# Optimization experiments

Hardware: AMD Instinct MI355X
Metric: run time of the kernel (lower is better)

## Reference

```python
import jax, jax.numpy as jnp
import numpy as np

N = 50000       # nodes
E = 800000      # edges
F_IN = 197      # node_feature_dim
H = 256         # hidden_dim
HEADS = 8
HD = H // HEADS # 32
L = 5           # num_layers
FF = 4 * H      # 1024
C = 2           # num_classes
ED = 2          # edge_feature_dim
SCALE = float(np.sqrt(HD))


def _ln(x, g, b):
    m = x.mean(-1, keepdims=True)
    v = ((x - m) ** 2).mean(-1, keepdims=True)
    return (x - m) / jnp.sqrt(v + 1e-5) * g + b


def setup_inputs() -> dict:
    key = jax.random.key(0)
    ks = iter(jax.random.split(key, 40))
    d = {}
    d["x"] = jax.random.normal(next(ks), (N, F_IN), dtype=jnp.float32)
    d["edge_index"] = jax.random.randint(next(ks), (2, E), 0, N, dtype=jnp.int64)
    d["edge_attr"] = jax.random.normal(next(ks), (E, ED), dtype=jnp.float32)
    xav = lambda k, sh: jax.random.normal(k, sh, dtype=jnp.float32) * float(np.sqrt(2.0 / (sh[-2] + sh[-1])))
    # input projection + LN
    d["in_W"] = xav(next(ks), (F_IN, H)); d["in_b"] = jnp.zeros((H,), jnp.float32)
    d["in_g"] = jnp.ones((H,), jnp.float32); d["in_bb"] = jnp.zeros((H,), jnp.float32)
    # stacked per-layer params (leading dim L)
    d["Wq"] = xav(next(ks), (L, H, H)); d["Wk"] = xav(next(ks), (L, H, H)); d["Wv"] = xav(next(ks), (L, H, H))
    d["We"] = xav(next(ks), (L, ED, HEADS)); d["be"] = jnp.zeros((L, HEADS), jnp.float32)
    d["Wo"] = xav(next(ks), (L, H, H)); d["bo"] = jnp.zeros((L, H), jnp.float32)
    d["ln1_g"] = jnp.ones((L, H), jnp.float32); d["ln1_b"] = jnp.zeros((L, H), jnp.float32)
    d["ln2_g"] = jnp.ones((L, H), jnp.float32); d["ln2_b"] = jnp.zeros((L, H), jnp.float32)
    d["f1_W"] = xav(next(ks), (L, H, FF)); d["f1_b"] = jnp.zeros((L, FF), jnp.float32)
    d["f2_W"] = xav(next(ks), (L, FF, H)); d["f2_b"] = jnp.zeros((L, H), jnp.float32)
    # classifier
    d["cls1_W"] = xav(next(ks), (H, H // 2)); d["cls1_b"] = jnp.zeros((H // 2,), jnp.float32)
    d["cls2_W"] = xav(next(ks), (H // 2, C)); d["cls2_b"] = jnp.zeros((C,), jnp.float32)
    return d


def _forward(x, edge_index, edge_attr, in_W, in_b, in_g, in_bb,
             Wq, Wk, Wv, We, be, Wo, bo, ln1_g, ln1_b, ln2_g, ln2_b,
             f1_W, f1_b, f2_W, f2_b, cls1_W, cls1_b, cls2_W, cls2_b):
    src, dst = edge_index[0], edge_index[1]  # message flows src -> dst
    h = jax.nn.gelu(_ln(x @ in_W + in_b, in_g, in_bb), approximate=False)

    def layer(h, p):
        wq, wk, wv, we, b_e, wo, b_o, g1, b1, g2, b2, w1, bf1, w2, bf2 = p
        hn = _ln(h, g1, b1)
        q = (hn @ wq).reshape(-1, HEADS, HD)
        k = (hn @ wk).reshape(-1, HEADS, HD)
        v = (hn @ wv).reshape(-1, HEADS, HD)
        edge_bias = edge_attr @ we + b_e                        # (E, HEADS)
        score = (q[dst] * k[src]).sum(-1) / SCALE + edge_bias   # (E, HEADS)
        # segment softmax over destination nodes
        mx = jax.ops.segment_max(score, dst, num_segments=N)
        mx = jnp.where(jnp.isfinite(mx), mx, 0.0)
        ex = jnp.exp(score - mx[dst])
        denom = jax.ops.segment_sum(ex, dst, num_segments=N)
        w = ex / (denom[dst] + 1e-16)                           # (E, HEADS)
        msg = w[:, :, None] * v[src]                            # (E, HEADS, HD)
        agg = jax.ops.segment_sum(msg.reshape(-1, H), dst, num_segments=N)
        out = agg @ wo + b_o
        out = _ln(out + h, g2, b2)                              # residual_proj = Identity
        ffn = jax.nn.gelu(out @ w1 + bf1, approximate=False) @ w2 + bf2
        return out + ffn, None

    params = (Wq, Wk, Wv, We, be, Wo, bo, ln1_g, ln1_b, ln2_g, ln2_b, f1_W, f1_b, f2_W, f2_b)
    h, _ = jax.lax.scan(layer, h, params)
    logits = jax.nn.gelu(h @ cls1_W + cls1_b, approximate=False) @ cls2_W + cls2_b
    probs = jax.nn.softmax(logits, axis=-1)
    return logits, probs


def reference(x, edge_index, edge_attr, in_W, in_b, in_g, in_bb,
              Wq, Wk, Wv, We, be, Wo, bo, ln1_g, ln1_b, ln2_g, ln2_b,
              f1_W, f1_b, f2_W, f2_b, cls1_W, cls1_b, cls2_W, cls2_b):
    return _forward(x, edge_index, edge_attr, in_W, in_b, in_g, in_bb,
                    Wq, Wk, Wv, We, be, Wo, bo, ln1_g, ln1_b, ln2_g, ln2_b,
                    f1_W, f1_b, f2_W, f2_b, cls1_W, cls1_b, cls2_W, cls2_b)
```

## Files before the change

kernel.cpp:

```cpp
#include <hip/hip_runtime.h>
#include <math.h>

#define NN 50000
#define NE 800000
#define FIN 197
#define KIN 224
#define H 256
#define HEADS 8
#define HD 32
#define LAYERS 5
#define FF 1024
#define INV_SCALE 0.17677669529663687f

typedef __attribute__((ext_vector_type(8))) short short8;
typedef __attribute__((ext_vector_type(4))) float f32x4;
typedef unsigned short ushort;

__device__ __forceinline__ float gelu_f(float x) {
    float x2 = x * x;
    float u = __builtin_fmaf(0.044715f * x2, x, x);
    float e = __builtin_amdgcn_exp2f(-2.3022075f * u);
    return x * __builtin_amdgcn_rcpf(1.0f + e);
}
__device__ __forceinline__ ushort f2b(float f) {
    unsigned u = __float_as_uint(f);
    u += 0x7fffu + ((u >> 16) & 1u);
    return (ushort)(u >> 16);
}
__device__ __forceinline__ float b2f(ushort b) {
    return __uint_as_float(((unsigned)b) << 16);
}
__device__ __forceinline__ float dot2b(unsigned a, unsigned b) {
    float a0 = __uint_as_float(a << 16), a1 = __uint_as_float(a & 0xffff0000u);
    float b0 = __uint_as_float(b << 16), b1 = __uint_as_float(b & 0xffff0000u);
    return a0 * b0 + a1 * b1;
}

__device__ __forceinline__ void load16_lds(const ushort* gp, ushort* lp) {
    __builtin_amdgcn_global_load_lds(
        (const __attribute__((address_space(1))) unsigned int*)gp,
        (__attribute__((address_space(3))) unsigned int*)lp,
        16, 0, 0);
}

__global__ __launch_bounds__(256) void gemm_bf16_kernel(
    const ushort* __restrict__ A, int lda,
    const ushort* __restrict__ Bt,
    const float* __restrict__ bias,
    const float* __restrict__ res, int ldr,
    float* __restrict__ Cf, ushort* __restrict__ Cb, int ldc,
    int n, int K, int act, int gx)
{
    __shared__ ushort As[2][128 * 32];
    __shared__ ushort Bs[2][64 * 32];
    int tid = threadIdx.x;
    int lane = tid & 63;
    int wave = tid >> 6;

    int tiles_y = (n + 127) >> 7;
    int lin = blockIdx.x;
    int gsz = gx * 8;
    int group = lin / gsz;
    int rem = lin - group * gsz;
    int rows_left = tiles_y - group * 8;
    int rg = rows_left < 8 ? rows_left : 8;
    int r = rem % rg;
    int c = rem / rg;
    int brow = (group * 8 + r) * 128;
    int bcol = c * 64;

    f32x4 acc[2][4] = {};
    int m0 = lane & 15;
    int rdc = ((lane >> 4) ^ ((lane >> 1) & 3)) * 8;

    int rA = lane >> 2;
    int c8s = (((lane & 3) ^ ((lane >> 3) & 3)) * 8);

    long arow0, arow1, brow0;
    {
        int gr0 = brow + wave * 32 + rA;        if (gr0 >= n) gr0 = n - 1;
        int gr1 = brow + wave * 32 + 16 + rA;   if (gr1 >= n) gr1 = n - 1;
        arow0 = (long)gr0 * lda;
        arow1 = (long)gr1 * lda;
        brow0 = (long)(bcol + wave * 16 + rA) * K;
    }
    int loA0 = (wave * 32) * 32;
    int loA1 = (wave * 32 + 16) * 32;
    int loB  = (wave * 16) * 32;

    int nt = K >> 5;
    load16_lds(A + arow0 + c8s, &As[0][loA0]);
    load16_lds(A + arow1 + c8s, &As[0][loA1]);
    load16_lds(Bt + brow0 + c8s, &Bs[0][loB]);
    __syncthreads();

    for (int t = 0; t < nt; ++t) {
        int p = t & 1;
        if (t + 1 < nt) {
            int k0 = (t + 1) << 5;
            load16_lds(A + arow0 + k0 + c8s, &As[p ^ 1][loA0]);
            load16_lds(A + arow1 + k0 + c8s, &As[p ^ 1][loA1]);
            load16_lds(Bt + brow0 + k0 + c8s, &Bs[p ^ 1][loB]);
        }
        short8 af[2], bfr[4];
        #pragma unroll
        for (int i = 0; i < 2; ++i)
            af[i] = *(const short8*)&As[p][(wave * 32 + i * 16 + m0) * 32 + rdc];
        #pragma unroll
        for (int j = 0; j < 4; ++j)
            bfr[j] = *(const short8*)&Bs[p][(j * 16 + m0) * 32 + rdc];
        #pragma unroll
        for (int i = 0; i < 2; ++i)
            #pragma unroll
            for (int j = 0; j < 4; ++j)
                acc[i][j] = __builtin_amdgcn_mfma_f32_16x16x32_bf16(af[i], bfr[j], acc[i][j], 0, 0, 0);
        __syncthreads();
    }

    float* ep0 = (float*)&As[0][wave * 1024];
    float* ep1 = (float*)&As[1][wave * 1024];
    int ccol = lane & 15;
    int crow0 = (lane >> 4) * 4;
    float* epw = (lane < 32) ? ep0 : ep1;
    #pragma unroll
    for (int i = 0; i < 2; ++i) {
        int rowbase = brow + wave * 32 + i * 16;
        #pragma unroll
        for (int rr = 0; rr < 4; ++rr) {
            int r8 = (crow0 + rr) & 7;
            #pragma unroll
            for (int j = 0; j < 4; ++j)
                epw[r8 * 64 + j * 16 + ccol] = acc[i][j][rr];
        }
        #pragma unroll
        for (int pass = 0; pass < 2; ++pass) {
            const float* ep = pass ? ep1 : ep0;
            #pragma unroll
            for (int k = 0; k < 2; ++k) {
                int idx = k * 64 + lane;
                int lr  = idx >> 4;
                int c4  = (idx & 15) * 4;
                int grow = rowbase + pass * 8 + lr;
                f32x4 v = *(const f32x4*)&ep[lr * 64 + c4];
                int gcol = bcol + c4;
                if (bias) {
                    float4 b4 = *(const float4*)(bias + gcol);
                    v[0] += b4.x; v[1] += b4.y; v[2] += b4.z; v[3] += b4.w;
                }
                if (act) {
                    v[0] = gelu_f(v[0]); v[1] = gelu_f(v[1]);
                    v[2] = gelu_f(v[2]); v[3] = gelu_f(v[3]);
                }
                if (grow < n) {
                    if (res) {
                        float4 r4 = *(const float4*)(res + (long)grow * ldr + gcol);
                        v[0] += r4.x; v[1] += r4.y; v[2] += r4.z; v[3] += r4.w;
                    }
                    if (Cf) *(f32x4*)(Cf + (long)grow * ldc + gcol) = v;
                    if (Cb) {
                        ushort4 ob = { f2b(v[0]), f2b(v[1]), f2b(v[2]), f2b(v[3]) };
                        *(ushort4*)(Cb + (long)grow * ldc + gcol) = ob;
                    }
                }
            }
        }
    }
}

__global__ __launch_bounds__(256) void ln256_kernel(
    const float* __restrict__ af, const ushort* __restrict__ ab,
    const float* __restrict__ res,
    const float* __restrict__ g, const float* __restrict__ bta,
    float* __restrict__ outf, ushort* __restrict__ outb, int n, int post_gelu)
{
    int row = blockIdx.x * 4 + (threadIdx.x >> 6);
    if (row >= n) return;
    int lane = threadIdx.x & 63;
    float4 v;
    if (af) {
        v = *(const float4*)(af + (long)row * H + lane * 4);
    } else {
        ushort4 vb = *(const ushort4*)(ab + (long)row * H + lane * 4);
        v.x = b2f(vb.x); v.y = b2f(vb.y); v.z = b2f(vb.z); v.w = b2f(vb.w);
    }
    if (res) {
        float4 r = *(const float4*)(res + (long)row * H + lane * 4);
        v.x += r.x; v.y += r.y; v.z += r.z; v.w += r.w;
    }
    float s = v.x + v.y + v.z + v.w;
    #pragma unroll
    for (int off = 1; off < 64; off <<= 1) s += __shfl_xor(s, off);
    float mean = s * (1.0f / H);
    float dx = v.x - mean, dy = v.y - mean, dz = v.z - mean, dw = v.w - mean;
    float qs = dx * dx + dy * dy + dz * dz + dw * dw;
    #pragma unroll
    for (int off = 1; off < 64; off <<= 1) qs += __shfl_xor(qs, off);
    float rstd = rsqrtf(qs * (1.0f / H) + 1e-5f);
    float4 gg = *(const float4*)(g + lane * 4);
    float4 bb = *(const float4*)(bta + lane * 4);
    float4 o;
    o.x = dx * rstd * gg.x + bb.x;
    o.y = dy * rstd * gg.y + bb.y;
    o.z = dz * rstd * gg.z + bb.z;
    o.w = dw * rstd * gg.w + bb.w;
    if (post_gelu) { o.x = gelu_f(o.x); o.y = gelu_f(o.y); o.z = gelu_f(o.z); o.w = gelu_f(o.w); }
    if (outf) *(float4*)(outf + (long)row * H + lane * 4) = o;
    if (outb) {
        ushort4 ob = { f2b(o.x), f2b(o.y), f2b(o.z), f2b(o.w) };
        *(ushort4*)(outb + (long)row * H + lane * 4) = ob;
    }
}

__global__ __launch_bounds__(256) void xcast_kernel(const float* __restrict__ x,
                                                    ushort* __restrict__ xb)
{
    long i = (long)blockIdx.x * 256 + threadIdx.x;
    if (i >= (long)NN * KIN) return;
    int n = (int)(i / KIN), c = (int)(i % KIN);
    xb[i] = (c < FIN) ? f2b(x[(long)n * FIN + c]) : (ushort)0;
}

__global__ __launch_bounds__(256) void wtin_kernel(const float* __restrict__ W,
                                                   ushort* __restrict__ Wt)
{
    int i = blockIdx.x * 256 + threadIdx.x;
    if (i >= 256 * KIN) return;
    int m = i / KIN, k = i % KIN;
    Wt[i] = (k < FIN) ? f2b(W[(long)k * H + m]) : (ushort)0;
}

__global__ __launch_bounds__(256) void wtqkv_kernel(
    const float* __restrict__ Wq, const float* __restrict__ Wk,
    const float* __restrict__ Wv, ushort* __restrict__ out)
{
    long i = (long)blockIdx.x * 256 + threadIdx.x;
    if (i >= (long)LAYERS * 768 * 256) return;
    int l = (int)(i / (768 * 256));
    int r = (int)(i % (768 * 256));
    int m = r >> 8, k = r & 255;
    const float* W = (m < 256) ? Wq : ((m < 512) ? Wk : Wv);
    out[i] = f2b(W[(long)l * 65536 + (long)k * 256 + (m & 255)]);
}

__global__ __launch_bounds__(256) void wtgen_kernel(
    const float* __restrict__ W, ushort* __restrict__ out, int L, int K, int M)
{
    long i = (long)blockIdx.x * 256 + threadIdx.x;
    if (i >= (long)L * K * M) return;
    int l = (int)(i / ((long)K * M));
    int r = (int)(i % ((long)K * M));
    int m = r / K, k = r % K;
    out[i] = f2b(W[(long)l * K * M + (long)k * M + m]);
}

__global__ __launch_bounds__(256) void deg_kernel(const int* __restrict__ dst,
                                                   int* __restrict__ deg)
{
    int e = blockIdx.x * 256 + threadIdx.x;
    if (e >= NE) return;
    atomicAdd(&deg[dst[e]], 1);
}

__global__ __launch_bounds__(256) void scan1_kernel(const int* __restrict__ deg,
                                                     int* __restrict__ rowptr,
                                                     int* __restrict__ bsum)
{
    __shared__ int buf[256];
    int tid = threadIdx.x;
    int i = blockIdx.x * 256 + tid;
    int v = (i < NN) ? deg[i] : 0;
    buf[tid] = v;
    __syncthreads();
    #pragma unroll
    for (int off = 1; off < 256; off <<= 1) {
        int t = (tid >= off) ? buf[tid - off] : 0;
        __syncthreads();
        buf[tid] += t;
        __syncthreads();
    }
    if (i < NN) rowptr[i] = buf[tid] - v;
    if (tid == 255) bsum[blockIdx.x] = buf[255];
}

__global__ __launch_bounds__(256) void scan2_kernel(int* __restrict__ bsum, int nb)
{
    __shared__ int buf[256];
    int tid = threadIdx.x;
    int v = (tid < nb) ? bsum[tid] : 0;
    buf[tid] = v;
    __syncthreads();
    #pragma unroll
    for (int off = 1; off < 256; off <<= 1) {
        int t = (tid >= off) ? buf[tid - off] : 0;
        __syncthreads();
        buf[tid] += t;
        __syncthreads();
    }
    if (tid < nb) bsum[tid] = buf[tid] - v;
}

__global__ __launch_bounds__(256) void scan3_kernel(int* __restrict__ rowptr,
                                                     const int* __restrict__ bsum)
{
    int i = blockIdx.x * 256 + threadIdx.x;
    if (i < NN) rowptr[i] += bsum[blockIdx.x];
    if (i == 0) rowptr[NN] = NE;
}

__global__ __launch_bounds__(256) void fill_kernel(
    const int* __restrict__ src, const int* __restrict__ dst,
    const float* __restrict__ ea, const int* __restrict__ rowptr,
    int* __restrict__ cursor, int* __restrict__ csr_src,
    float2* __restrict__ csr_ea)
{
    int e = blockIdx.x * 256 + threadIdx.x;
    if (e >= NE) return;
    int d = dst[e];
    int pos = atomicAdd(&cursor[d], 1);
    int j = rowptr[d] + pos;
    csr_src[j] = src[e];
    csr_ea[j] = *(const float2*)(ea + 2 * e);
}

#define LOADE(idx, kbuf, vbuf, ebuf)                                   \
    { int s_ = csr_src[idx]; ebuf = csr_ea[idx];                       \
      const ushort* kr_ = qkv + (long)s_ * 768 + 256;                  \
      kbuf = *(const uint2*)(kr_ + lane * 4);                          \
      vbuf = *(const uint2*)(kr_ + 256 + lane * 4); }

#define PAIR(k1, v1, e1, k2, v2, e2)                                               \
    { float p1 = dot2b(q2.x, (k1).x) + dot2b(q2.y, (k1).y);                        \
      float p2 = dot2b(q2.x, (k2).x) + dot2b(q2.y, (k2).y);                        \
      p1 += __shfl_xor(p1, 1);  p2 += __shfl_xor(p2, 1);                           \
      p1 += __shfl_xor(p1, 2);  p2 += __shfl_xor(p2, 2);                           \
      p1 += __shfl_xor(p1, 4);  p2 += __shfl_xor(p2, 4);                           \
      float s1 = p1 * c1 + (e1).x * w0 + (e1).y * w1 + bb;                         \
      float s2 = p2 * c1 + (e2).x * w0 + (e2).y * w1 + bb;                         \
      float mp = fmaxf(s1, s2);                                                    \
      float x1 = __builtin_amdgcn_exp2f(s1 - mp);                                  \
      float x2 = __builtin_amdgcn_exp2f(s2 - mp);                                  \
      float lp = x1 + x2;                                                          \
      float b0 = x1 * __uint_as_float((v1).x << 16)         + x2 * __uint_as_float((v2).x << 16);          \
      float b1 = x1 * __uint_as_float((v1).x & 0xffff0000u) + x2 * __uint_as_float((v2).x & 0xffff0000u);  \
      float b2 = x1 * __uint_as_float((v1).y << 16)         + x2 * __uint_as_float((v2).y << 16);          \
      float b3 = x1 * __uint_as_float((v1).y & 0xffff0000u) + x2 * __uint_as_float((v2).y & 0xffff0000u);  \
      float mn = fmaxf(m, mp);                                                     \
      float so = __builtin_amdgcn_exp2f(m - mn);                                   \
      float sp = __builtin_amdgcn_exp2f(mp - mn);                                  \
      l  = l  * so + lp * sp;                                                      \
      a0 = a0 * so + b0 * sp;                                                      \
      a1 = a1 * so + b1 * sp;                                                      \
      a2 = a2 * so + b2 * sp;                                                      \
      a3 = a3 * so + b3 * sp;                                                      \
      m = mn; }

#define SINGLE(kb, vb, eb)                                                         \
    { float p1 = dot2b(q2.x, (kb).x) + dot2b(q2.y, (kb).y);                        \
      p1 += __shfl_xor(p1, 1);                                                     \
      p1 += __shfl_xor(p1, 2);                                                     \
      p1 += __shfl_xor(p1, 4);                                                     \
      float s1 = p1 * c1 + (eb).x * w0 + (eb).y * w1 + bb;                         \
      float mn = fmaxf(m, s1);                                                     \
      float so = __builtin_amdgcn_exp2f(m - mn);                                   \
      float e_ = __builtin_amdgcn_exp2f(s1 - mn);                                  \
      l  = l  * so + e_;                                                           \
      a0 = a0 * so + e_ * __uint_as_float((vb).x << 16);                           \
      a1 = a1 * so + e_ * __uint_as_float((vb).x & 0xffff0000u);                   \
      a2 = a2 * so + e_ * __uint_as_float((vb).y << 16);                           \
      a3 = a3 * so + e_ * __uint_as_float((vb).y & 0xffff0000u);                   \
      m = mn; }

__global__ __launch_bounds__(256) void attn_kernel(
    const ushort* __restrict__ qkv,
    const int* __restrict__ rowptr, const int* __restrict__ csr_src,
    const float2* __restrict__ csr_ea,
    const float* __restrict__ We, const float* __restrict__ be,
    ushort* __restrict__ aggb)
{
    int node = blockIdx.x * 4 + (threadIdx.x >> 6);
    if (node >= NN) return;
    int lane = threadIdx.x & 63;
    int h = lane >> 3;
    const float L2E = 1.4426950408889634f;
    float w0 = We[h] * L2E, w1 = We[8 + h] * L2E, bb = be[h] * L2E;
    const float c1 = INV_SCALE * L2E;

    uint2 q2 = *(const uint2*)(qkv + (long)node * 768 + lane * 4);
    int jbeg = rowptr[node], jend = rowptr[node + 1];

    float m = -1e30f, l = 0.f;
    float a0 = 0.f, a1 = 0.f, a2 = 0.f, a3 = 0.f;

    uint2 k0v = {0,0}, v0v = {0,0}, k1v = {0,0}, v1v = {0,0};
    uint2 k2v = {0,0}, v2v = {0,0}, k3v = {0,0}, v3v = {0,0};
    float2 e0v = {0.f,0.f}, e1v = {0.f,0.f}, e2v = {0.f,0.f}, e3v = {0.f,0.f};

    if (jbeg + 0 < jend) LOADE(jbeg + 0, k0v, v0v, e0v);
    if (jbeg + 1 < jend) LOADE(jbeg + 1, k1v, v1v, e1v);
    if (jbeg + 2 < jend) LOADE(jbeg + 2, k2v, v2v, e2v);
    if (jbeg + 3 < jend) LOADE(jbeg + 3, k3v, v3v, e3v);

    int j = jbeg;
    for (; j + 3 < jend; j += 4) {
        PAIR(k0v, v0v, e0v, k1v, v1v, e1v);
        if (j + 4 < jend) LOADE(j + 4, k0v, v0v, e0v);
        if (j + 5 < jend) LOADE(j + 5, k1v, v1v, e1v);
        PAIR(k2v, v2v, e2v, k3v, v3v, e3v);
        if (j + 6 < jend) LOADE(j + 6, k2v, v2v, e2v);
        if (j + 7 < jend) LOADE(j + 7, k3v, v3v, e3v);
    }
    int rleft = jend - j;
    if (rleft >= 2) PAIR(k0v, v0v, e0v, k1v, v1v, e1v);
    if (rleft == 3) SINGLE(k2v, v2v, e2v);
    if (rleft == 1) SINGLE(k0v, v0v, e0v);

    float inv = 1.0f / (l + 1e-16f);
    ushort4 o = { f2b(a0 * inv), f2b(a1 * inv), f2b(a2 * inv), f2b(a3 * inv) };
    *(ushort4*)(aggb + (long)node * 256 + lane * 4) = o;
}

__global__ __launch_bounds__(256) void cls_kernel(
    const float* __restrict__ t1, const float* __restrict__ W,
    const float* __restrict__ b, float* __restrict__ out)
{
    int i = blockIdx.x * 256 + threadIdx.x;
    if (i >= NN) return;
    const float* tp = t1 + (long)i * 128;
    float a0 = 0.f, a1 = 0.f;
    #pragma unroll
    for (int j = 0; j < 128; j += 4) {
        float4 t = *(const float4*)(tp + j);
        a0 += t.x * W[(j + 0) * 2] + t.y * W[(j + 1) * 2] + t.z * W[(j + 2) * 2] + t.w * W[(j + 3) * 2];
        a1 += t.x * W[(j + 0) * 2 + 1] + t.y * W[(j + 1) * 2 + 1] + t.z * W[(j + 2) * 2 + 1] + t.w * W[(j + 3) * 2 + 1];
    }
    float l0 = a0 + b[0], l1 = a1 + b[1];
    out[(long)i * 2 + 0] = l0;
    out[(long)i * 2 + 1] = l1;
    float mx = fmaxf(l0, l1);
    float p0 = expf(l0 - mx), p1 = expf(l1 - mx);
    float sden = p0 + p1;
    out[2L * NN + (long)i * 2 + 0] = p0 / sden;
    out[2L * NN + (long)i * 2 + 1] = p1 / sden;
}

extern "C" void kernel_launch(void* const* d_in, const int* in_sizes, int n_in,
                              void* d_out, int out_size, void* d_ws, size_t ws_size,
                              hipStream_t stream) {
    const float* x      = (const float*)d_in[0];
    const int*   ei     = (const int*)d_in[1];
    const float* ea     = (const float*)d_in[2];
    const float* in_W   = (const float*)d_in[3];
    const float* in_b   = (const float*)d_in[4];
    const float* in_g   = (const float*)d_in[5];
    const float* in_bb  = (const float*)d_in[6];
    const float* Wq     = (const float*)d_in[7];
    const float* Wk     = (const float*)d_in[8];
    const float* Wv     = (const float*)d_in[9];
    const float* We     = (const float*)d_in[10];
    const float* be     = (const float*)d_in[11];
    const float* Wo     = (const float*)d_in[12];
    const float* bo     = (const float*)d_in[13];
    const float* ln1_g  = (const float*)d_in[14];
    const float* ln1_b  = (const float*)d_in[15];
    const float* ln2_g  = (const float*)d_in[16];
    const float* ln2_b  = (const float*)d_in[17];
    const float* f1_W   = (const float*)d_in[18];
    const float* f1_b   = (const float*)d_in[19];
    const float* f2_W   = (const float*)d_in[20];
    const float* f2_b   = (const float*)d_in[21];
    const float* cls1_W = (const float*)d_in[22];
    const float* cls1_b = (const float*)d_in[23];
    const float* cls2_W = (const float*)d_in[24];
    const float* cls2_b = (const float*)d_in[25];
    float* out = (float*)d_out;

    const int* src = ei;
    const int* dst = ei + NE;

    char* w = (char*)d_ws;
    float* B0 = (float*)w;            w += (size_t)NN * H * 4;
    ushort* hb = (ushort*)w;          w += (size_t)NN * H * 2;
    char* pool = w;                   w += (size_t)NN * 1024 * 2;
    ushort* qkv  = (ushort*)pool;
    ushort* aggb = (ushort*)(pool + (size_t)NN * 768 * 2);
    float*  tproj = (float*)pool;
    ushort* xb   = (ushort*)(pool + (size_t)NN * H * 4);
    ushort* tb   = (ushort*)pool;
    float*  t1   = (float*)pool;
    int* deg    = (int*)w;            w += (size_t)NN * 4;
    int* cursor = (int*)w;            w += (size_t)NN * 4;
    int* rowptr = (int*)w;            w += (size_t)(NN + 2) * 4;
    int* bsum   = (int*)w;            w += 1024;
    int* csr_src = (int*)w;           w += (size_t)NE * 4;
    float2* csr_ea = (float2*)w;      w += (size_t)NE * 8;
    ushort* wqkv_t = (ushort*)w;      w += (size_t)LAYERS * 768 * 256 * 2;
    ushort* wo_t  = (ushort*)w;       w += (size_t)LAYERS * 65536 * 2;
    ushort* f1_t  = (ushort*)w;       w += (size_t)LAYERS * 262144 * 2;
    ushort* f2_t  = (ushort*)w;       w += (size_t)LAYERS * 262144 * 2;
    ushort* c1_t  = (ushort*)w;       w += (size_t)32768 * 2;
    ushort* inw_t = (ushort*)w;       w += (size_t)256 * KIN * 2;

    dim3 blk(256);
    const int ln_grid = (NN + 3) / 4;
    const int e_grid = (NE + 255) / 256;
    const int n_grid = (NN + 255) / 256;
    const int ty = (NN + 127) / 128;

    hipMemsetAsync(deg, 0, (size_t)NN * 4, stream);
    hipMemsetAsync(cursor, 0, (size_t)NN * 4, stream);
    deg_kernel<<<e_grid, blk, 0, stream>>>(dst, deg);
    scan1_kernel<<<n_grid, blk, 0, stream>>>(deg, rowptr, bsum);
    scan2_kernel<<<1, blk, 0, stream>>>(bsum, n_grid);
    scan3_kernel<<<n_grid, blk, 0, stream>>>(rowptr, bsum);
    fill_kernel<<<e_grid, blk, 0, stream>>>(src, dst, ea, rowptr, cursor, csr_src, csr_ea);

    wtqkv_kernel<<<(int)(((long)LAYERS * 768 * 256 + 255) / 256), blk, 0, stream>>>(Wq, Wk, Wv, wqkv_t);
    wtgen_kernel<<<(int)(((long)LAYERS * 65536 + 255) / 256), blk, 0, stream>>>(Wo, wo_t, LAYERS, 256, 256);
    wtgen_kernel<<<(int)(((long)LAYERS * 262144 + 255) / 256), blk, 0, stream>>>(f1_W, f1_t, LAYERS, 256, 1024);
    wtgen_kernel<<<(int)(((long)LAYERS * 262144 + 255) / 256), blk, 0, stream>>>(f2_W, f2_t, LAYERS, 1024, 256);
    wtgen_kernel<<<(32768 + 255) / 256, blk, 0, stream>>>(cls1_W, c1_t, 1, 256, 128);
    wtin_kernel<<<(256 * KIN + 255) / 256, blk, 0, stream>>>(in_W, inw_t);

    xcast_kernel<<<(int)(((long)NN * KIN + 255) / 256), blk, 0, stream>>>(x, xb);
    {
        gemm_bf16_kernel<<<4 * ty, blk, 0, stream>>>(xb, KIN, inw_t, in_b, nullptr, 0,
                                                     tproj, nullptr, H, NN, KIN, 0, 4);
        ln256_kernel<<<ln_grid, blk, 0, stream>>>(tproj, nullptr, nullptr, in_g, in_bb, B0, nullptr, NN, 1);
    }

    for (int l = 0; l < LAYERS; ++l) {
        const float* we  = We + (long)l * 16;
        const float* bel = be + (long)l * 8;
        const float* bol = bo + (long)l * H;
        const float* g1 = ln1_g + (long)l * H;
        const float* b1 = ln1_b + (long)l * H;
        const float* g2 = ln2_g + (long)l * H;
        const float* b2 = ln2_b + (long)l * H;
        const float* bf1 = f1_b + (long)l * FF;
        const float* bf2 = f2_b + (long)l * H;

        ln256_kernel<<<ln_grid, blk, 0, stream>>>(B0, nullptr, nullptr, g1, b1, nullptr, hb, NN, 0);

        gemm_bf16_kernel<<<12 * ty, blk, 0, stream>>>(hb, H, wqkv_t + (long)l * 768 * 256,
            nullptr, nullptr, 0, nullptr, qkv, 768, NN, H, 0, 12);
        attn_kernel<<<(NN + 3) / 4, blk, 0, stream>>>(qkv, rowptr, csr_src, csr_ea, we, bel, aggb);

        gemm_bf16_kernel<<<4 * ty, blk, 0, stream>>>(aggb, H, wo_t + (long)l * 65536,
            bol, nullptr, 0, nullptr, qkv, H, NN, H, 0, 4);
        ln256_kernel<<<ln_grid, blk, 0, stream>>>(nullptr, qkv, B0, g2, b2, B0, hb, NN, 0);

        gemm_bf16_kernel<<<16 * ty, blk, 0, stream>>>(hb, H, f1_t + (long)l * 262144,
            bf1, nullptr, 0, nullptr, tb, FF, NN, H, 1, 16);
        gemm_bf16_kernel<<<4 * ty, blk, 0, stream>>>(tb, FF, f2_t + (long)l * 262144,
            bf2, B0, H, B0, (l == LAYERS - 1) ? hb : nullptr, H, NN, FF, 0, 4);
    }

    {
        gemm_bf16_kernel<<<2 * ty, blk, 0, stream>>>(hb, H, c1_t, cls1_b, nullptr, 0,
                                                     t1, nullptr, 128, NN, H, 1, 2);
        cls_kernel<<<n_grid, blk, 0, stream>>>(t1, cls2_W, cls2_b, out);
    }
}
```

Baseline: 2.103 ms.

## Widen GEMM block tile to 128x128 and restructure epilogue staging

```diff
diff --git a/kernel.cpp b/kernel.cpp
--- a/kernel.cpp
+++ b/kernel.cpp
@@ -52,7 +52,7 @@
     int n, int K, int act, int gx)
 {
     __shared__ ushort As[2][128 * 32];
-    __shared__ ushort Bs[2][64 * 32];
+    __shared__ ushort Bs[2][128 * 32];
     int tid = threadIdx.x;
     int lane = tid & 63;
     int wave = tid >> 6;
@@ -67,103 +67,102 @@
     int r = rem % rg;
     int c = rem / rg;
     int brow = (group * 8 + r) * 128;
-    int bcol = c * 64;
-
-    f32x4 acc[2][4] = {};
+    int bcol = c * 128;
+
+    f32x4 acc[2][8] = {};
     int m0 = lane & 15;
     int rdc = ((lane >> 4) ^ ((lane >> 1) & 3)) * 8;
 
     int rA = lane >> 2;
     int c8s = (((lane & 3) ^ ((lane >> 3) & 3)) * 8);
 
-    long arow0, arow1, brow0;
+    long arow0, arow1, brow0, brow1;
     {
         int gr0 = brow + wave * 32 + rA;        if (gr0 >= n) gr0 = n - 1;
         int gr1 = brow + wave * 32 + 16 + rA;   if (gr1 >= n) gr1 = n - 1;
         arow0 = (long)gr0 * lda;
         arow1 = (long)gr1 * lda;
-        brow0 = (long)(bcol + wave * 16 + rA) * K;
-    }
-    int loA0 = (wave * 32) * 32;
-    int loA1 = (wave * 32 + 16) * 32;
-    int loB  = (wave * 16) * 32;
+        brow0 = (long)(bcol + wave * 32 + rA) * K;
+        brow1 = (long)(bcol + wave * 32 + 16 + rA) * K;
+    }
+    int lo0 = (wave * 32) * 32;
+    int lo1 = (wave * 32 + 16) * 32;
 
     int nt = K >> 5;
-    load16_lds(A + arow0 + c8s, &As[0][loA0]);
-    load16_lds(A + arow1 + c8s, &As[0][loA1]);
-    load16_lds(Bt + brow0 + c8s, &Bs[0][loB]);
+    load16_lds(A + arow0 + c8s, &As[0][lo0]);
+    load16_lds(A + arow1 + c8s, &As[0][lo1]);
+    load16_lds(Bt + brow0 + c8s, &Bs[0][lo0]);
+    load16_lds(Bt + brow1 + c8s, &Bs[0][lo1]);
     __syncthreads();
 
     for (int t = 0; t < nt; ++t) {
         int p = t & 1;
         if (t + 1 < nt) {
             int k0 = (t + 1) << 5;
-            load16_lds(A + arow0 + k0 + c8s, &As[p ^ 1][loA0]);
-            load16_lds(A + arow1 + k0 + c8s, &As[p ^ 1][loA1]);
-            load16_lds(Bt + brow0 + k0 + c8s, &Bs[p ^ 1][loB]);
+            load16_lds(A + arow0 + k0 + c8s, &As[p ^ 1][lo0]);
+            load16_lds(A + arow1 + k0 + c8s, &As[p ^ 1][lo1]);
+            load16_lds(Bt + brow0 + k0 + c8s, &Bs[p ^ 1][lo0]);
+            load16_lds(Bt + brow1 + k0 + c8s, &Bs[p ^ 1][lo1]);
         }
-        short8 af[2], bfr[4];
+        short8 af[2], bfr[8];
         #pragma unroll
         for (int i = 0; i < 2; ++i)
             af[i] = *(const short8*)&As[p][(wave * 32 + i * 16 + m0) * 32 + rdc];
         #pragma unroll
-        for (int j = 0; j < 4; ++j)
+        for (int j = 0; j < 8; ++j)
             bfr[j] = *(const short8*)&Bs[p][(j * 16 + m0) * 32 + rdc];
         #pragma unroll
         for (int i = 0; i < 2; ++i)
             #pragma unroll
-            for (int j = 0; j < 4; ++j)
+            for (int j = 0; j < 8; ++j)
                 acc[i][j] = __builtin_amdgcn_mfma_f32_16x16x32_bf16(af[i], bfr[j], acc[i][j], 0, 0, 0);
         __syncthreads();
     }
 
-    float* ep0 = (float*)&As[0][wave * 1024];
-    float* ep1 = (float*)&As[1][wave * 1024];
+    float* ch0 = (float*)&As[0][wave * 1024];
+    float* ch1 = (float*)&As[1][wave * 1024];
+    float* ch2 = (float*)&Bs[0][wave * 1024];
+    float* ch3 = (float*)&Bs[1][wave * 1024];
     int ccol = lane & 15;
-    int crow0 = (lane >> 4) * 4;
-    float* epw = (lane < 32) ? ep0 : ep1;
+    int mych = lane >> 4;
+    float* wch = (mych == 0) ? ch0 : ((mych == 1) ? ch1 : ((mych == 2) ? ch2 : ch3));
+    int gcol = bcol + (lane & 31) * 4;
     #pragma unroll
     for (int i = 0; i < 2; ++i) {
         int rowbase = brow + wave * 32 + i * 16;
         #pragma unroll
-        for (int rr = 0; rr < 4; ++rr) {
-            int r8 = (crow0 + rr) & 7;
+        for (int rr = 0; rr < 4; ++rr)
             #pragma unroll
-            for (int j = 0; j < 4; ++j)
-                epw[r8 * 64 + j * 16 + ccol] = acc[i][j][rr];
-        }
+            for (int j = 0; j < 8; ++j)
+                wch[rr * 128 + j * 16 + ccol] = acc[i][j][rr];
         #pragma unroll
-        for (int pass = 0; pass < 2; ++pass) {
-            const float* ep = pass ? ep1 : ep0;
-            #pragma unroll
-            for (int k = 0; k < 2; ++k) {
-                int idx = k * 64 + lane;
-                int lr  = idx >> 4;
-                int c4  = (idx & 15) * 4;
-                int grow = rowbase + pass * 8 + lr;
-                f32x4 v = *(const f32x4*)&ep[lr * 64 + c4];
-                int gcol = bcol + c4;
-                if (bias) {
-                    float4 b4 = *(const float4*)(bias + gcol);
-                    v[0] += b4.x; v[1] += b4.y; v[2] += b4.z; v[3] += b4.w;
+        for (int k = 0; k < 8; ++k) {
+            const float* rch = ((k >> 1) == 0) ? ch0 :
+                               (((k >> 1) == 1) ? ch1 :
+                               (((k >> 1) == 2) ? ch2 : ch3));
+            f32x4 v = *(const f32x4*)&rch[(((k & 1) * 64) + lane) * 4];
+            int grow = rowbase + 2 * k + (lane >> 5);
+            if (bias) {
+                float4 b4 = *(const float4*)(bias + gcol);
+                v[0] += b4.x; v[1] += b4.y; v[2] += b4.z; v[3] += b4.w;
+            }
+            if (act) {
+                v[0] = gelu_f(v[0]); v[1] = gelu_f(v[1]);
+                v[2] = gelu_f(v[2]); v[3] = gelu_f(v[3]);
+            }
+            if (grow < n) {
+                if (res) {
+                    float4 r4 = *(const float4*)(res + (long)grow * ldr + gcol);
+                    v[0] += r4.x; v[1] += r4.y; v[2] += r4.z; v[3] += r4.w;
                 }
-                if (act) {
-                    v[0] = gelu_f(v[0]); v[1] = gelu_f(v[1]);
-                    v[2] = gelu_f(v[2]); v[3] = gelu_f(v[3]);
-                }
-                if (grow < n) {
-                    if (res) {
-                        float4 r4 = *(const float4*)(res + (long)grow * ldr + gcol);
-                        v[0] += r4.x; v[1] += r4.y; v[2] += r4.z; v[3] += r4.w;
-                    }
-                    if (Cf) *(f32x4*)(Cf + (long)grow * ldc + gcol) = v;
-                    if (Cb) {
-                        ushort4 ob = { f2b(v[0]), f2b(v[1]), f2b(v[2]), f2b(v[3]) };
-                        *(ushort4*)(Cb + (long)grow * ldc + gcol) = ob;
-                    }
+                if (Cf) *(f32x4*)(Cf + (long)grow * ldc + gcol) = v;
+                if (Cb) {
+                    ushort4 ob = { f2b(v[0]), f2b(v[1]), f2b(v[2]), f2b(v[3]) };
+                    *(ushort4*)(Cb + (long)grow * ldc + gcol) = ob;
                 }
             }
         }
+        if (i == 0) __syncthreads();
     }
 }
 
@@ -523,8 +522,8 @@
 
     xcast_kernel<<<(int)(((long)NN * KIN + 255) / 256), blk, 0, stream>>>(x, xb);
     {
-        gemm_bf16_kernel<<<4 * ty, blk, 0, stream>>>(xb, KIN, inw_t, in_b, nullptr, 0,
-                                                     tproj, nullptr, H, NN, KIN, 0, 4);
+        gemm_bf16_kernel<<<2 * ty, blk, 0, stream>>>(xb, KIN, inw_t, in_b, nullptr, 0,
+                                                     tproj, nullptr, H, NN, KIN, 0, 2);
         ln256_kernel<<<ln_grid, blk, 0, stream>>>(tproj, nullptr, nullptr, in_g, in_bb, B0, nullptr, NN, 1);
     }
 
@@ -541,23 +540,23 @@
 
         ln256_kernel<<<ln_grid, blk, 0, stream>>>(B0, nullptr, nullptr, g1, b1, nullptr, hb, NN, 0);
 
-        gemm_bf16_kernel<<<12 * ty, blk, 0, stream>>>(hb, H, wqkv_t + (long)l * 768 * 256,
-            nullptr, nullptr, 0, nullptr, qkv, 768, NN, H, 0, 12);
+        gemm_bf16_kernel<<<6 * ty, blk, 0, stream>>>(hb, H, wqkv_t + (long)l * 768 * 256,
+            nullptr, nullptr, 0, nullptr, qkv, 768, NN, H, 0, 6);
         attn_kernel<<<(NN + 3) / 4, blk, 0, stream>>>(qkv, rowptr, csr_src, csr_ea, we, bel, aggb);
 
-        gemm_bf16_kernel<<<4 * ty, blk, 0, stream>>>(aggb, H, wo_t + (long)l * 65536,
-            bol, nullptr, 0, nullptr, qkv, H, NN, H, 0, 4);
+        gemm_bf16_kernel<<<2 * ty, blk, 0, stream>>>(aggb, H, wo_t + (long)l * 65536,
+            bol, nullptr, 0, nullptr, qkv, H, NN, H, 0, 2);
         ln256_kernel<<<ln_grid, blk, 0, stream>>>(nullptr, qkv, B0, g2, b2, B0, hb, NN, 0);
 
-        gemm_bf16_kernel<<<16 * ty, blk, 0, stream>>>(hb, H, f1_t + (long)l * 262144,
-            bf1, nullptr, 0, nullptr, tb, FF, NN, H, 1, 16);
-        gemm_bf16_kernel<<<4 * ty, blk, 0, stream>>>(tb, FF, f2_t + (long)l * 262144,
-            bf2, B0, H, B0, (l == LAYERS - 1) ? hb : nullptr, H, NN, FF, 0, 4);
+        gemm_bf16_kernel<<<8 * ty, blk, 0, stream>>>(hb, H, f1_t + (long)l * 262144,
+            bf1, nullptr, 0, nullptr, tb, FF, NN, H, 1, 8);
+        gemm_bf16_kernel<<<2 * ty, blk, 0, stream>>>(tb, FF, f2_t + (long)l * 262144,
+            bf2, B0, H, B0, (l == LAYERS - 1) ? hb : nullptr, H, NN, FF, 0, 2);
     }
 
     {
-        gemm_bf16_kernel<<<2 * ty, blk, 0, stream>>>(hb, H, c1_t, cls1_b, nullptr, 0,
-                                                     t1, nullptr, 128, NN, H, 1, 2);
+        gemm_bf16_kernel<<<1 * ty, blk, 0, stream>>>(hb, H, c1_t, cls1_b, nullptr, 0,
+                                                     t1, nullptr, 128, NN, H, 1, 1);
         cls_kernel<<<n_grid, blk, 0, stream>>>(t1, cls2_W, cls2_b, out);
     }
 }
```

Result: no change. 2.074 ms (-1.4%).
